# Optimization experiments

Hardware: AMD Instinct MI355X
Metric: run time of the kernel (lower is better)

The kernel has to match this reference:

```python
import jax, jax.numpy as jnp
import numpy as np
import math

N, E, C, NB, NEL, NG = 8192, 131072, 64, 8, 4, 16
R_MAX, AVG_NEI, P_CUT, NL, SH = 5.0, 16.0, 6, 2, 16


def _sph(u):
    # real spherical harmonics l=0..3, component normalization (sum_m Y_lm^2 = 2l+1 on unit sphere)
    x, y, z = u[:, 0], u[:, 1], u[:, 2]
    s3, s15, s5 = math.sqrt(3.0), math.sqrt(15.0), math.sqrt(5.0)
    s105, s7 = math.sqrt(105.0), math.sqrt(7.0)
    c35, c21 = math.sqrt(35.0 / 8.0), math.sqrt(21.0 / 8.0)
    Y = [jnp.ones_like(x),
         s3 * x, s3 * y, s3 * z,
         s15 * x * y, s15 * y * z, 0.5 * s5 * (3 * z * z - 1), s15 * x * z, 0.5 * s15 * (x * x - y * y),
         c35 * y * (3 * x * x - y * y), s105 * x * y * z, c21 * y * (5 * z * z - 1),
         0.5 * s7 * (5 * z ** 3 - 3 * z), c21 * x * (5 * z * z - 1),
         0.5 * s105 * z * (x * x - y * y), c35 * x * (x * x - 3 * y * y)]
    return jnp.stack(Y, axis=-1)  # [E,16]


def _bessel(r):
    k = jnp.arange(1, NB + 1, dtype=r.dtype)
    return math.sqrt(2.0 / R_MAX) * jnp.sin(k * jnp.pi * r[:, None] / R_MAX) / r[:, None]


def _poly_cutoff(r):
    p = float(P_CUT)
    x = r / R_MAX
    f = (1.0 - 0.5 * (p + 1) * (p + 2) * x ** p + p * (p + 2) * x ** (p + 1)
         - 0.5 * p * (p + 1) * x ** (p + 2))
    return f * (x < 1.0)


def setup_inputs() -> dict:
    key = jax.random.key(0)
    ks = jax.random.split(key, 16)
    sc = lambda fan: 1.0 / math.sqrt(fan)
    return {
        "pos": 2.0 * jax.random.normal(ks[0], (N, 3), jnp.float32),
        "atom_types": jax.random.randint(ks[1], (N,), 0, NEL),
        "edge_index": jax.random.randint(ks[2], (2, E), 0, N),
        "batch": jnp.sort(jax.random.randint(ks[3], (N,), 0, NG)),
        "W_embed": jax.random.normal(ks[4], (NEL, C), jnp.float32),
        "W_r1": sc(NB) * jax.random.normal(ks[5], (NL, NB, 64), jnp.float32),
        "W_r2": sc(64) * jax.random.normal(ks[6], (NL, 64, 64), jnp.float32),
        "W_r3": sc(64) * jax.random.normal(ks[7], (NL, 64, C), jnp.float32),
        "W_sc": sc(C) * jax.random.normal(ks[8], (NL, NEL, C, C), jnp.float32),
        "w_prod": 0.5 * jax.random.normal(ks[9], (NL, NEL, 4), jnp.float32),
        "w_ro0": sc(C) * jax.random.normal(ks[10], (C,), jnp.float32),
        "W_ro1a": sc(C) * jax.random.normal(ks[11], (C, 16), jnp.float32),
        "w_ro1b": sc(16) * jax.random.normal(ks[12], (16,), jnp.float32),
    }


def reference(pos, atom_types, edge_index, batch, W_embed, W_r1, W_r2, W_r3,
              W_sc, w_prod, w_ro0, W_ro1a, w_ro1b):
    src, dst = edge_index[0], edge_index[1]
    vec = pos[dst] - pos[src]                      # [E,3]
    r = jnp.sqrt(jnp.sum(vec * vec, -1) + 1e-12)   # [E]
    Y = _sph(vec / r[:, None])                     # [E,SH]
    edge_feats = _bessel(r) * _poly_cutoff(r)[:, None]  # [E,NB]
    h = W_embed[atom_types]                        # one-hot @ W == lookup, [N,C]
    energies = [jnp.zeros((NG,), pos.dtype)]       # pair_repulsion disabled
    for i in range(NL):
        Rw = jax.nn.silu(edge_feats @ W_r1[i])
        Rw = jax.nn.silu(Rw @ W_r2[i])
        Rw = Rw @ W_r3[i]                          # radial MLP weights [E,C]
        # gather-TP-scatter: message [E,C,SH] -> node A [N,C,SH]
        m = (Rw * h[src])[:, :, None] * Y[:, None, :]
        A = jax.ops.segment_sum(m.reshape(E, C * SH), dst,
                                num_segments=N).reshape(N, C, SH) / AVG_NEI
        sc_feat = jnp.einsum('nc,ncd->nd', h, W_sc[i][atom_types])  # element-dep skip
        inv = jnp.stack([A[:, :, 0],
                         jnp.sum(A[:, :, 1:4] ** 2, -1),
                         jnp.sum(A[:, :, 4:9] ** 2, -1),
                         jnp.sum(A[:, :, 9:16] ** 2, -1)], axis=-1)  # [N,C,4]
        h = jnp.einsum('ncj,nj->nc', inv, w_prod[i][atom_types]) + sc_feat
        if i < NL - 1:
            e_node = h @ w_ro0                     # linear readout
        else:
            e_node = jax.nn.silu(h @ W_ro1a) @ w_ro1b  # gated MLP readout
        energies.append(jax.ops.segment_sum(e_node, batch, num_segments=NG))
    contributions = jnp.stack(energies, -1)        # [NG, NL+1]
    return jnp.sum(contributions, -1)              # total energy per graph
```

## Files before the change

kernel.cpp:

```cpp
#include <hip/hip_runtime.h>
#include <hip/hip_bf16.h>
#include <math.h>

#define N_NODES 8192
#define N_EDGES 131072
#define NGRP 16
#define NLAY 2
#define NELM 4
constexpr float INV_AVG = 1.0f / 16.0f;
constexpr float PI_F = 3.14159265358979323846f;

#define CV_POS   0
#define CV_EMB   24576
#define CV_SC    42240
#define CV_PROD  75008
#define CV_RO0   75040
#define CV_RO1A  75104
#define CV_RO1B  76128
#define CVT_N    76144

#define SWZ_PER_L 10240
#define SWZ_N     20480

#define B_CVT  230
#define B_SWZ  80
#define B_HIST 512
#define CVT_WORK 58736

typedef __hip_bfloat16 bf16;
typedef __attribute__((ext_vector_type(8))) short bf16x8;
typedef __attribute__((ext_vector_type(4))) float f32x4;

__device__ __forceinline__ float silu_f(float x){ return x / (1.0f + __expf(-x)); }
__device__ __forceinline__ float bfbits2f(unsigned short u){
  return __uint_as_float(((unsigned)u) << 16);
}
__device__ __forceinline__ void unpack2(unsigned u, float& lo, float& hi){
  lo = __uint_as_float(u << 16);
  hi = __uint_as_float(u & 0xffff0000u);
}
__device__ __forceinline__ short f2bs(float v){
  union { bf16 b; short s; } u; u.b = __float2bfloat16(v); return u.s;
}
__device__ __forceinline__ float ldf(const void* p, int i, int flag){
  if (flag) return bfbits2f(((const unsigned short*)p)[i]);
  return ((const float*)p)[i];
}
__device__ __forceinline__ int detect_fl(const void* pos){
  int lane = threadIdx.x & 63;
  const unsigned short* u = (const unsigned short*)pos;
  float va = bfbits2f(u[2*lane]), vb = bfbits2f(u[2*lane+1]);
  bool bad = !(fabsf(va) <= 1000.0f) || !(fabsf(vb) <= 1000.0f);
  return (__ballot(bad) == 0ull) ? 1 : 0;
}
__device__ __forceinline__ void WSYNC(){ __builtin_amdgcn_wave_barrier(); }

__device__ __forceinline__ void gl_lds4(const void* g, void* l){
  __builtin_amdgcn_global_load_lds(
      (const __attribute__((address_space(1))) unsigned*)g,
      (__attribute__((address_space(3))) unsigned*)l, 4, 0, 0);
}
__device__ __forceinline__ void gl_lds16(const void* g, void* l){
  __builtin_amdgcn_global_load_lds(
      (const __attribute__((address_space(1))) unsigned*)g,
      (__attribute__((address_space(3))) unsigned*)l, 16, 0, 0);
}

__global__ void k_setup1(const void* __restrict__ pos, const void* __restrict__ Wemb,
                         const void* __restrict__ Wsc, const void* __restrict__ wprod,
                         const void* __restrict__ wro0, const void* __restrict__ Wro1a,
                         const void* __restrict__ wro1b, const void* __restrict__ Wr1,
                         const void* __restrict__ Wr2, const void* __restrict__ Wr3,
                         const int* __restrict__ dstp, float* __restrict__ cv,
                         short* __restrict__ swz, int* __restrict__ deg){
  int b = blockIdx.x, tix = threadIdx.x;
  if (b >= B_CVT + B_SWZ){
    int e = (b - B_CVT - B_SWZ)*256 + tix;
    atomicAdd(&deg[dstp[e]], 1);
    return;
  }
  int fl = detect_fl(pos);
  if (b < B_CVT){
    int i = b*256 + tix;
    if (i < 24576){ cv[CV_POS + i] = ldf(pos, i, fl); return; }
    if (i < 24832){ int j=i-24576; cv[CV_EMB + j] = ldf(Wemb, j, fl); return; }
    if (i < 57600){ int j=i-24832; cv[CV_SC  + j] = ldf(Wsc,  j, fl); return; }
    if (i < 57632){ int j=i-57600; cv[CV_PROD+ j] = ldf(wprod,j, fl); return; }
    if (i < 57696){ int j=i-57632; cv[CV_RO0 + j] = ldf(wro0, j, fl); return; }
    if (i < 58720){ int j=i-57696; cv[CV_RO1A+ j] = ldf(Wro1a,j, fl); return; }
    if (i < CVT_WORK){ int j=i-58720; cv[CV_RO1B+ j] = ldf(wro1b,j, fl); return; }
    return;
  }
  int i = (b - B_CVT)*256 + tix;
  int l = i / SWZ_PER_L, w = i % SWZ_PER_L;
  float v;
  if (w < 2048){
    int t = w >> 9, q = (w >> 7) & 3, n = (w >> 3) & 15, j = w & 7;
    int k = q*8 + j;
    v = (k < 8) ? ldf(Wr1, l*512 + k*64 + t*16 + n, fl) : 0.0f;
  } else if (w < 6144){
    int w2 = w - 2048;
    int nt = w2 >> 10, kt = (w2 >> 9) & 1, q = (w2 >> 7) & 3, n = (w2 >> 3) & 15, j = w2 & 7;
    int k = kt*32 + q*8 + j;
    v = ldf(Wr2, l*4096 + k*64 + nt*16 + n, fl);
  } else {
    int w3 = w - 6144;
    int nt = w3 >> 10, kt = (w3 >> 9) & 1, q = (w3 >> 7) & 3, n = (w3 >> 3) & 15, j = w3 & 7;
    int k = kt*32 + q*8 + j;
    v = ldf(Wr3, l*4096 + k*64 + nt*16 + n, fl);
  }
  swz[i] = f2bs(v);
}

__global__ void k_setup2(const int* __restrict__ deg, int* __restrict__ row_start,
                         int* __restrict__ cursor, const int* __restrict__ types,
                         const float* __restrict__ cvemb, float* __restrict__ h,
                         float* __restrict__ ene){
  if (blockIdx.x == 0){
    __shared__ int lds[1024];
    int t = threadIdx.x;
    if (t < NGRP) ene[t] = 0.0f;
    int v[8]; int tot = 0;
#pragma unroll
    for (int k = 0; k < 8; k++){ v[k] = deg[t*8+k]; tot += v[k]; }
    lds[t] = tot; __syncthreads();
    for (int off = 1; off < 1024; off <<= 1){
      int x = (t >= off) ? lds[t-off] : 0;
      __syncthreads();
      lds[t] += x;
      __syncthreads();
    }
    int base = lds[t] - tot;
#pragma unroll
    for (int k = 0; k < 8; k++){ row_start[t*8+k] = base; cursor[t*8+k] = base; base += v[k]; }
    if (t == 1023) row_start[N_NODES] = base;
  } else {
    int i = (blockIdx.x - 1)*1024 + threadIdx.x;
    int n = i >> 6, c = i & 63;
    h[i] = cvemb[types[n]*64 + c];
  }
}

__global__ void k_fillgeom(const int* __restrict__ ei, int* __restrict__ cursor,
                           const float* __restrict__ posf, int* __restrict__ sslot,
                           unsigned short* __restrict__ Yb, float* __restrict__ rbuf){
  int e = blockIdx.x*256 + threadIdx.x;
  int s = ei[e], d = ei[N_EDGES + e];
  int slot = atomicAdd(&cursor[d], 1);
  sslot[slot] = s;
  float vx = posf[d*3+0] - posf[s*3+0];
  float vy = posf[d*3+1] - posf[s*3+1];
  float vz = posf[d*3+2] - posf[s*3+2];
  float r = sqrtf(vx*vx + vy*vy + vz*vz + 1e-12f);
  float ir = 1.0f / r;
  float x = vx*ir, y = vy*ir, z = vz*ir;
  const float s3 = 1.7320508075688772f, s15 = 3.872983346207417f, s5 = 2.23606797749979f;
  const float s105 = 10.246950765959598f, s7 = 2.6457513110645907f;
  const float c35 = 2.091650066335189f, c21 = 1.6201851746019651f;
  float x2 = x*x, y2 = y*y, z2 = z*z;
  float ys[16] = {
    1.0f, s3*x, s3*y, s3*z,
    s15*x*y, s15*y*z, 0.5f*s5*(3.0f*z2-1.0f), s15*x*z,
    0.5f*s15*(x2-y2), c35*y*(3.0f*x2-y2), s105*x*y*z, c21*y*(5.0f*z2-1.0f),
    0.5f*s7*(5.0f*z2*z-3.0f*z), c21*x*(5.0f*z2-1.0f), 0.5f*s105*z*(x2-y2),
    c35*x*(x2-3.0f*y2) };
  union { bf16 b[16]; uint4 u[2]; } pk;
#pragma unroll
  for (int k = 0; k < 16; k++) pk.b[k] = __float2bfloat16(ys[k]);
  uint4* yp = (uint4*)(Yb + (size_t)slot*16);
  yp[0] = pk.u[0];
  yp[1] = pk.u[1];
  rbuf[slot] = r;
}

#define ROWS 72
__global__ void __launch_bounds__(256) k_mlp2(const float* __restrict__ rbuf,
        const short* __restrict__ sw, bf16* __restrict__ Rwb){
  __shared__ short lds[4][16*ROWS];
  int tix = threadIdx.x;
  int wv = tix >> 6, lane = tix & 63;
  int q = lane >> 4, nn = lane & 15;
  int ebase = blockIdx.x*64 + wv*16;

  float r = rbuf[ebase + nn];
  float xc = r * 0.2f;
  float f = 0.0f;
  if (xc < 1.0f){
    float x3 = xc*xc*xc, x6 = x3*x3, x7 = x6*xc, x8 = x7*xc;
    f = 1.0f - 28.0f*x6 + 48.0f*x7 - 21.0f*x8;
  }
  float bs = 0.6324555320336759f * f / r;
  float t0 = PI_F * r * 0.2f;
  float ef[8];
#pragma unroll
  for (int k = 0; k < 8; k++) ef[k] = bs * __sinf((float)(k+1) * t0);

  bf16x8 af1 = {0,0,0,0,0,0,0,0};
  if (q == 0){
#pragma unroll
    for (int j = 0; j < 8; j++) af1[j] = f2bs(ef[j]);
  }
  short* A = lds[wv];
  int row = lane >> 2, c4 = lane & 3;

  for (int l = 0; l < NLAY; l++){
    const bf16x8* S1 = (const bf16x8*)(sw + l*SWZ_PER_L);
    const bf16x8* S2 = (const bf16x8*)(sw + l*SWZ_PER_L + 2048);
    const bf16x8* S3 = (const bf16x8*)(sw + l*SWZ_PER_L + 6144);
    f32x4 acc[4];
#pragma unroll
    for (int t = 0; t < 4; t++){
      bf16x8 b = S1[t*64 + q*16 + nn];
      f32x4 z = {0.f,0.f,0.f,0.f};
      acc[t] = __builtin_amdgcn_mfma_f32_16x16x32_bf16(af1, b, z, 0, 0, 0);
    }
#pragma unroll
    for (int t = 0; t < 4; t++)
#pragma unroll
      for (int rg = 0; rg < 4; rg++)
        A[(q*4+rg)*ROWS + t*16 + nn] = f2bs(silu_f(acc[t][rg]));
    WSYNC();

    bf16x8 a0 = *(const bf16x8*)&A[nn*ROWS + 0*32 + q*8];
    bf16x8 a1 = *(const bf16x8*)&A[nn*ROWS + 1*32 + q*8];
    WSYNC();
#pragma unroll
    for (int t = 0; t < 4; t++){
      f32x4 z = {0.f,0.f,0.f,0.f};
      bf16x8 b0 = S2[t*128 + 0*64 + q*16 + nn];
      bf16x8 b1 = S2[t*128 + 1*64 + q*16 + nn];
      z = __builtin_amdgcn_mfma_f32_16x16x32_bf16(a0, b0, z, 0, 0, 0);
      z = __builtin_amdgcn_mfma_f32_16x16x32_bf16(a1, b1, z, 0, 0, 0);
      acc[t] = z;
    }
#pragma unroll
    for (int t = 0; t < 4; t++)
#pragma unroll
      for (int rg = 0; rg < 4; rg++)
        A[(q*4+rg)*ROWS + t*16 + nn] = f2bs(silu_f(acc[t][rg]));
    WSYNC();

    a0 = *(const bf16x8*)&A[nn*ROWS + 0*32 + q*8];
    a1 = *(const bf16x8*)&A[nn*ROWS + 1*32 + q*8];
    WSYNC();
#pragma unroll
    for (int t = 0; t < 4; t++){
      f32x4 z = {0.f,0.f,0.f,0.f};
      bf16x8 b0 = S3[t*128 + 0*64 + q*16 + nn];
      bf16x8 b1 = S3[t*128 + 1*64 + q*16 + nn];
      z = __builtin_amdgcn_mfma_f32_16x16x32_bf16(a0, b0, z, 0, 0, 0);
      z = __builtin_amdgcn_mfma_f32_16x16x32_bf16(a1, b1, z, 0, 0, 0);
      acc[t] = z;
    }
#pragma unroll
    for (int t = 0; t < 4; t++)
#pragma unroll
      for (int rg = 0; rg < 4; rg++)
        A[(q*4+rg)*ROWS + t*16 + nn] = f2bs(acc[t][rg]);
    WSYNC();

    uint4 u0 = *(const uint4*)&A[row*ROWS + c4*16];
    uint4 u1 = *(const uint4*)&A[row*ROWS + c4*16 + 8];
    uint4* gp = (uint4*)((unsigned short*)Rwb + (size_t)l*N_EDGES*64
                         + ((size_t)(ebase + row))*64 + c4*16);
    gp[0] = u0;
    gp[1] = u1;
    WSYNC();
  }
}

template<int LAYER_KIND>
__global__ void __launch_bounds__(256) k_gu(const bf16* __restrict__ Rwb,
        const float* __restrict__ h_old, float* __restrict__ h_new,
        const unsigned short* __restrict__ Yb, const int* __restrict__ row_start,
        const int* __restrict__ sslot,
        const int* __restrict__ types, const float* __restrict__ Wsc,
        const float* __restrict__ wprod, const float* __restrict__ wro0,
        const float* __restrict__ Wro1a, const float* __restrict__ wro1b,
        const int* __restrict__ batch, float* __restrict__ ene){
  __shared__ __align__(16) float          hS[4][16][64];
  __shared__ __align__(16) unsigned short rwS[4][16][64];
  __shared__ __align__(16) unsigned short yS[4][16][16];
  __shared__ float ebins[NGRP];
  __shared__ float hn_l[4][64];
  int tix = threadIdx.x;
  if (tix < NGRP) ebins[tix] = 0.0f;
  __syncthreads();
  int wv = tix >> 6, lane = tix & 63;
  int n = blockIdx.x * 4 + wv;
  int beg = row_start[n], end = row_start[n + 1];
  const unsigned short* RW = (const unsigned short*)Rwb;

  float acc[16];
#pragma unroll
  for (int s = 0; s < 16; s++) acc[s] = 0.0f;

  for (int cb = beg; cb < end; cb += 16){
    int cnt = min(16, end - cb);
    WSYNC();
    int sv = sslot[min(cb + (lane & 15), N_EDGES - 1)];
    const char* rwsrc = (const char*)RW + (size_t)cb*128 + lane*16;
    gl_lds16(rwsrc,        &rwS[wv][0][0]);
    gl_lds16(rwsrc + 1024, &rwS[wv][8][0]);
    const char* ysrc = (const char*)Yb + (size_t)cb*32 + lane*4;
    gl_lds4(ysrc,       &yS[wv][0][0]);
    gl_lds4(ysrc + 256, &yS[wv][8][0]);
    for (int i = 0; i < cnt; i++){
      int src = __builtin_amdgcn_readlane(sv, i);
      gl_lds4(h_old + (size_t)src*64 + lane, &hS[wv][i][0]);
    }
    asm volatile("s_waitcnt vmcnt(0)" ::: "memory");
    __builtin_amdgcn_sched_barrier(0);
    for (int i = 0; i < cnt; i++){
      float g = hS[wv][i][lane] * bfbits2f(rwS[wv][i][lane]);
      const uint4* yq = (const uint4*)&yS[wv][i][0];
      uint4 ya = yq[0], yb = yq[1];
      float lo, hi;
      unpack2(ya.x, lo, hi); acc[0]  += g*lo; acc[1]  += g*hi;
      unpack2(ya.y, lo, hi); acc[2]  += g*lo; acc[3]  += g*hi;
      unpack2(ya.z, lo, hi); acc[4]  += g*lo; acc[5]  += g*hi;
      unpack2(ya.w, lo, hi); acc[6]  += g*lo; acc[7]  += g*hi;
      unpack2(yb.x, lo, hi); acc[8]  += g*lo; acc[9]  += g*hi;
      unpack2(yb.y, lo, hi); acc[10] += g*lo; acc[11] += g*hi;
      unpack2(yb.z, lo, hi); acc[12] += g*lo; acc[13] += g*hi;
      unpack2(yb.w, lo, hi); acc[14] += g*lo; acc[15] += g*hi;
    }
  }
#pragma unroll
  for (int s = 0; s < 16; s++) acc[s] *= INV_AVG;

  int ty = __builtin_amdgcn_readfirstlane(types[n]);
  const float* Ws = Wsc + (size_t)ty*4096;
  float sc0 = 0.f, sc1 = 0.f, sc2 = 0.f, sc3 = 0.f;
#pragma unroll
  for (int c = 0; c < 64; c += 4){
    sc0 += h_old[(size_t)n*64 + c+0] * Ws[(c+0)*64 + lane];
    sc1 += h_old[(size_t)n*64 + c+1] * Ws[(c+1)*64 + lane];
    sc2 += h_old[(size_t)n*64 + c+2] * Ws[(c+2)*64 + lane];
    sc3 += h_old[(size_t)n*64 + c+3] * Ws[(c+3)*64 + lane];
  }
  float sc = (sc0 + sc1) + (sc2 + sc3);

  float inv0 = acc[0];
  float inv1 = acc[1]*acc[1] + acc[2]*acc[2] + acc[3]*acc[3];
  float inv2 = acc[4]*acc[4] + acc[5]*acc[5] + acc[6]*acc[6] + acc[7]*acc[7]
             + acc[8]*acc[8];
  float inv3 = acc[9]*acc[9] + acc[10]*acc[10] + acc[11]*acc[11] + acc[12]*acc[12]
             + acc[13]*acc[13] + acc[14]*acc[14] + acc[15]*acc[15];
  const float* wp = wprod + ty*4;
  float hn = inv0*wp[0] + inv1*wp[1] + inv2*wp[2] + inv3*wp[3] + sc;
  h_new[(size_t)n*64 + lane] = hn;

  float ev;
  if (LAYER_KIND == 0){
    float p = hn * wro0[lane];
#pragma unroll
    for (int off = 32; off >= 1; off >>= 1) p += __shfl_xor(p, off, 64);
    ev = p;
  } else {
    hn_l[wv][lane] = hn;
    int j = lane & 15;
    float pj = 0.0f;
#pragma unroll
    for (int c = 0; c < 64; c++)
      pj += hn_l[wv][c] * Wro1a[c*16 + j];
    float evj = silu_f(pj) * wro1b[j];
    evj += __shfl_xor(evj, 8, 64);
    evj += __shfl_xor(evj, 4, 64);
    evj += __shfl_xor(evj, 2, 64);
    evj += __shfl_xor(evj, 1, 64);
    ev = evj;
  }
  if (lane == 0) atomicAdd(&ebins[batch[n]], ev);
  __syncthreads();
  if (tix < NGRP){
    float v = ebins[tix];
    if (v != 0.0f) atomicAdd(&ene[tix], v);
  }
}

__global__ void k_out(const float* __restrict__ ene, const void* __restrict__ pos,
                      void* __restrict__ out){
  int fl = detect_fl(pos);
  int t = threadIdx.x;
  if (t < NGRP){
    if (fl) ((bf16*)out)[t] = __float2bfloat16(ene[t]);
    else    ((float*)out)[t] = ene[t];
  }
}

static inline size_t rup(size_t x){ return (x + 255) & ~(size_t)255; }

extern "C" void kernel_launch(void* const* d_in, const int* in_sizes, int n_in,
                              void* d_out, int out_size, void* d_ws, size_t ws_size,
                              hipStream_t stream) {
  const void* pos   = d_in[0];
  const int*  types = (const int*)d_in[1];
  const int*  ei    = (const int*)d_in[2];
  const int*  batch = (const int*)d_in[3];
  const void* Wemb  = d_in[4];
  const void* Wr1   = d_in[5];
  const void* Wr2   = d_in[6];
  const void* Wr3   = d_in[7];
  const void* Wsc   = d_in[8];
  const void* wprod = d_in[9];
  const void* wro0  = d_in[10];
  const void* Wro1a = d_in[11];
  const void* wro1b = d_in[12];

  char* w = (char*)d_ws;
  float* cv       = (float*)w; w += rup((size_t)CVT_N*4);
  short* swz      = (short*)w; w += rup((size_t)SWZ_N*2);
  float* ene      = (float*)w; w += 256;
  int*   deg      = (int*)  w; w += rup((size_t)N_NODES*4);
  int*   row_start= (int*)  w; w += rup((size_t)(N_NODES+1)*4);
  int*   cursor   = (int*)  w; w += rup((size_t)N_NODES*4);
  int*   sslot    = (int*)  w; w += rup((size_t)N_EDGES*4);
  float* h0       = (float*)w; w += rup((size_t)N_NODES*64*4);
  float* h1       = (float*)w; w += rup((size_t)N_NODES*64*4);
  float* rbuf     = (float*)w; w += rup((size_t)N_EDGES*4);
  unsigned short* Yb = (unsigned short*)w; w += rup((size_t)N_EDGES*16*2);
  bf16*  Rwb      = (bf16*) w; w += rup((size_t)NLAY*N_EDGES*64*2);
  w += 4096;

  hipMemsetAsync(deg, 0, N_NODES*4, stream);

  const int* dstp = ei + N_EDGES;
  k_setup1<<<B_CVT + B_SWZ + B_HIST, 256, 0, stream>>>(
      pos, Wemb, Wsc, wprod, wro0, Wro1a, wro1b, Wr1, Wr2, Wr3, dstp, cv, swz, deg);
  k_setup2<<<1 + (N_NODES*64)/1024, 1024, 0, stream>>>(
      deg, row_start, cursor, types, cv + CV_EMB, h0, ene);
  k_fillgeom<<<N_EDGES/256, 256, 0, stream>>>(ei, cursor, cv + CV_POS, sslot, Yb, rbuf);
  k_mlp2<<<N_EDGES/64, 256, 0, stream>>>(rbuf, swz, Rwb);

  k_gu<0><<<N_NODES/4, 256, 0, stream>>>(Rwb, h0, h1, Yb,
      row_start, sslot, types, cv + CV_SC, cv + CV_PROD,
      cv + CV_RO0, cv + CV_RO1A, cv + CV_RO1B, batch, ene);
  k_gu<1><<<N_NODES/4, 256, 0, stream>>>(Rwb + (size_t)N_EDGES*64, h1, h0, Yb,
      row_start, sslot, types, cv + CV_SC + (size_t)NELM*4096, cv + CV_PROD + NELM*4,
      cv + CV_RO0, cv + CV_RO1A, cv + CV_RO1B, batch, ene);

  k_out<<<1, 64, 0, stream>>>(ene, pos, d_out);
}
```

Measured before the change: 203.0 us.

## Fuse radial MLP into gather-update kernel, dropping the Rw edge buffer

Removes the separate radial MLP kernel and its bf16 per-edge weight buffer. Each gather kernel now recomputes the MFMA-based radial MLP for the block's edge chunk and multiplies it into the gathered neighbour features in LDS. The four waves cooperatively process 64-edge chunks covering the block's four nodes, with block-level syncs between stages. This trades global write/read traffic of the Rw buffer for redundant basis computation and extra __syncthreads per chunk.

```diff
diff --git a/kernel.cpp b/kernel.cpp
--- a/kernel.cpp
+++ b/kernel.cpp
@@ -59,11 +59,6 @@
   __builtin_amdgcn_global_load_lds(
       (const __attribute__((address_space(1))) unsigned*)g,
       (__attribute__((address_space(3))) unsigned*)l, 4, 0, 0);
-}
-__device__ __forceinline__ void gl_lds16(const void* g, void* l){
-  __builtin_amdgcn_global_load_lds(
-      (const __attribute__((address_space(1))) unsigned*)g,
-      (__attribute__((address_space(3))) unsigned*)l, 16, 0, 0);
 }
 
 __global__ void k_setup1(const void* __restrict__ pos, const void* __restrict__ Wemb,
@@ -174,103 +169,9 @@
 }
 
 #define ROWS 72
-__global__ void __launch_bounds__(256) k_mlp2(const float* __restrict__ rbuf,
-        const short* __restrict__ sw, bf16* __restrict__ Rwb){
-  __shared__ short lds[4][16*ROWS];
-  int tix = threadIdx.x;
-  int wv = tix >> 6, lane = tix & 63;
-  int q = lane >> 4, nn = lane & 15;
-  int ebase = blockIdx.x*64 + wv*16;
-
-  float r = rbuf[ebase + nn];
-  float xc = r * 0.2f;
-  float f = 0.0f;
-  if (xc < 1.0f){
-    float x3 = xc*xc*xc, x6 = x3*x3, x7 = x6*xc, x8 = x7*xc;
-    f = 1.0f - 28.0f*x6 + 48.0f*x7 - 21.0f*x8;
-  }
-  float bs = 0.6324555320336759f * f / r;
-  float t0 = PI_F * r * 0.2f;
-  float ef[8];
-#pragma unroll
-  for (int k = 0; k < 8; k++) ef[k] = bs * __sinf((float)(k+1) * t0);
-
-  bf16x8 af1 = {0,0,0,0,0,0,0,0};
-  if (q == 0){
-#pragma unroll
-    for (int j = 0; j < 8; j++) af1[j] = f2bs(ef[j]);
-  }
-  short* A = lds[wv];
-  int row = lane >> 2, c4 = lane & 3;
-
-  for (int l = 0; l < NLAY; l++){
-    const bf16x8* S1 = (const bf16x8*)(sw + l*SWZ_PER_L);
-    const bf16x8* S2 = (const bf16x8*)(sw + l*SWZ_PER_L + 2048);
-    const bf16x8* S3 = (const bf16x8*)(sw + l*SWZ_PER_L + 6144);
-    f32x4 acc[4];
-#pragma unroll
-    for (int t = 0; t < 4; t++){
-      bf16x8 b = S1[t*64 + q*16 + nn];
-      f32x4 z = {0.f,0.f,0.f,0.f};
-      acc[t] = __builtin_amdgcn_mfma_f32_16x16x32_bf16(af1, b, z, 0, 0, 0);
-    }
-#pragma unroll
-    for (int t = 0; t < 4; t++)
-#pragma unroll
-      for (int rg = 0; rg < 4; rg++)
-        A[(q*4+rg)*ROWS + t*16 + nn] = f2bs(silu_f(acc[t][rg]));
-    WSYNC();
-
-    bf16x8 a0 = *(const bf16x8*)&A[nn*ROWS + 0*32 + q*8];
-    bf16x8 a1 = *(const bf16x8*)&A[nn*ROWS + 1*32 + q*8];
-    WSYNC();
-#pragma unroll
-    for (int t = 0; t < 4; t++){
-      f32x4 z = {0.f,0.f,0.f,0.f};
-      bf16x8 b0 = S2[t*128 + 0*64 + q*16 + nn];
-      bf16x8 b1 = S2[t*128 + 1*64 + q*16 + nn];
-      z = __builtin_amdgcn_mfma_f32_16x16x32_bf16(a0, b0, z, 0, 0, 0);
-      z = __builtin_amdgcn_mfma_f32_16x16x32_bf16(a1, b1, z, 0, 0, 0);
-      acc[t] = z;
-    }
-#pragma unroll
-    for (int t = 0; t < 4; t++)
-#pragma unroll
-      for (int rg = 0; rg < 4; rg++)
-        A[(q*4+rg)*ROWS + t*16 + nn] = f2bs(silu_f(acc[t][rg]));
-    WSYNC();
-
-    a0 = *(const bf16x8*)&A[nn*ROWS + 0*32 + q*8];
-    a1 = *(const bf16x8*)&A[nn*ROWS + 1*32 + q*8];
-    WSYNC();
-#pragma unroll
-    for (int t = 0; t < 4; t++){
-      f32x4 z = {0.f,0.f,0.f,0.f};
-      bf16x8 b0 = S3[t*128 + 0*64 + q*16 + nn];
-      bf16x8 b1 = S3[t*128 + 1*64 + q*16 + nn];
-      z = __builtin_amdgcn_mfma_f32_16x16x32_bf16(a0, b0, z, 0, 0, 0);
-      z = __builtin_amdgcn_mfma_f32_16x16x32_bf16(a1, b1, z, 0, 0, 0);
-      acc[t] = z;
-    }
-#pragma unroll
-    for (int t = 0; t < 4; t++)
-#pragma unroll
-      for (int rg = 0; rg < 4; rg++)
-        A[(q*4+rg)*ROWS + t*16 + nn] = f2bs(acc[t][rg]);
-    WSYNC();
-
-    uint4 u0 = *(const uint4*)&A[row*ROWS + c4*16];
-    uint4 u1 = *(const uint4*)&A[row*ROWS + c4*16 + 8];
-    uint4* gp = (uint4*)((unsigned short*)Rwb + (size_t)l*N_EDGES*64
-                         + ((size_t)(ebase + row))*64 + c4*16);
-    gp[0] = u0;
-    gp[1] = u1;
-    WSYNC();
-  }
-}
-
 template<int LAYER_KIND>
-__global__ void __launch_bounds__(256) k_gu(const bf16* __restrict__ Rwb,
+__global__ void __launch_bounds__(256) k_gu(const short* __restrict__ sw,
+        const float* __restrict__ rbuf,
         const float* __restrict__ h_old, float* __restrict__ h_new,
         const unsigned short* __restrict__ Yb, const int* __restrict__ row_start,
         const int* __restrict__ sslot,
@@ -278,53 +179,146 @@
         const float* __restrict__ wprod, const float* __restrict__ wro0,
         const float* __restrict__ Wro1a, const float* __restrict__ wro1b,
         const int* __restrict__ batch, float* __restrict__ ene){
-  __shared__ __align__(16) float          hS[4][16][64];
-  __shared__ __align__(16) unsigned short rwS[4][16][64];
-  __shared__ __align__(16) unsigned short yS[4][16][16];
+  __shared__ __align__(16) float hS[64][64];
+  __shared__ __align__(16) unsigned short yS[64][16];
+  __shared__ short A_[4][16*ROWS];
   __shared__ float ebins[NGRP];
   __shared__ float hn_l[4][64];
   int tix = threadIdx.x;
   if (tix < NGRP) ebins[tix] = 0.0f;
   __syncthreads();
   int wv = tix >> 6, lane = tix & 63;
-  int n = blockIdx.x * 4 + wv;
-  int beg = row_start[n], end = row_start[n + 1];
-  const unsigned short* RW = (const unsigned short*)Rwb;
+  int q = lane >> 4, nn = lane & 15;
+  int n0 = blockIdx.x * 4;
+  int n  = n0 + wv;
+  int s0 = row_start[n0], sEnd = row_start[n0 + 4];
+  int my_beg = row_start[n], my_end = row_start[n + 1];
+  short* A = A_[wv];
+  int row = lane >> 2, c4 = lane & 3;
+
+  const bf16x8* S1 = (const bf16x8*)(sw);
+  const bf16x8* S2 = (const bf16x8*)(sw + 2048);
+  const bf16x8* S3 = (const bf16x8*)(sw + 6144);
 
   float acc[16];
 #pragma unroll
   for (int s = 0; s < 16; s++) acc[s] = 0.0f;
 
-  for (int cb = beg; cb < end; cb += 16){
-    int cnt = min(16, end - cb);
-    WSYNC();
-    int sv = sslot[min(cb + (lane & 15), N_EDGES - 1)];
-    const char* rwsrc = (const char*)RW + (size_t)cb*128 + lane*16;
-    gl_lds16(rwsrc,        &rwS[wv][0][0]);
-    gl_lds16(rwsrc + 1024, &rwS[wv][8][0]);
-    const char* ysrc = (const char*)Yb + (size_t)cb*32 + lane*4;
-    gl_lds4(ysrc,       &yS[wv][0][0]);
-    gl_lds4(ysrc + 256, &yS[wv][8][0]);
-    for (int i = 0; i < cnt; i++){
+  for (int cb = s0; cb < sEnd; cb += 64){
+    int wbase = cb + wv*16;
+    int wcnt  = min(16, max(0, sEnd - wbase));
+    int sv = sslot[min(wbase + nn, N_EDGES - 1)];
+    for (int i = 0; i < wcnt; i++){
       int src = __builtin_amdgcn_readlane(sv, i);
-      gl_lds4(h_old + (size_t)src*64 + lane, &hS[wv][i][0]);
+      gl_lds4(h_old + (size_t)src*64 + lane, &hS[wv*16 + i][0]);
+    }
+    if (wcnt > 0){
+      const char* ysrc = (const char*)Yb + (size_t)wbase*32 + lane*4;
+      gl_lds4(ysrc,       &yS[wv*16][0]);
+      gl_lds4(ysrc + 256, &yS[wv*16 + 8][0]);
+    }
+    {
+      float r = rbuf[min(wbase + nn, N_EDGES - 1)];
+      float xc = r * 0.2f;
+      float f = 0.0f;
+      if (xc < 1.0f){
+        float x3 = xc*xc*xc, x6 = x3*x3, x7 = x6*xc, x8 = x7*xc;
+        f = 1.0f - 28.0f*x6 + 48.0f*x7 - 21.0f*x8;
+      }
+      float bs = 0.6324555320336759f * f / r;
+      float t0 = PI_F * r * 0.2f;
+      bf16x8 af1 = {0,0,0,0,0,0,0,0};
+      if (q == 0){
+#pragma unroll
+        for (int j = 0; j < 8; j++) af1[j] = f2bs(bs * __sinf((float)(j+1) * t0));
+      }
+      f32x4 macc[4];
+#pragma unroll
+      for (int t = 0; t < 4; t++){
+        bf16x8 b = S1[t*64 + q*16 + nn];
+        f32x4 z = {0.f,0.f,0.f,0.f};
+        macc[t] = __builtin_amdgcn_mfma_f32_16x16x32_bf16(af1, b, z, 0, 0, 0);
+      }
+#pragma unroll
+      for (int t = 0; t < 4; t++)
+#pragma unroll
+        for (int rg = 0; rg < 4; rg++)
+          A[(q*4+rg)*ROWS + t*16 + nn] = f2bs(silu_f(macc[t][rg]));
+      WSYNC();
+      bf16x8 a0 = *(const bf16x8*)&A[nn*ROWS + 0*32 + q*8];
+      bf16x8 a1 = *(const bf16x8*)&A[nn*ROWS + 1*32 + q*8];
+      WSYNC();
+#pragma unroll
+      for (int t = 0; t < 4; t++){
+        f32x4 z = {0.f,0.f,0.f,0.f};
+        bf16x8 b0 = S2[t*128 + 0*64 + q*16 + nn];
+        bf16x8 b1 = S2[t*128 + 1*64 + q*16 + nn];
+        z = __builtin_amdgcn_mfma_f32_16x16x32_bf16(a0, b0, z, 0, 0, 0);
+        z = __builtin_amdgcn_mfma_f32_16x16x32_bf16(a1, b1, z, 0, 0, 0);
+        macc[t] = z;
+      }
+#pragma unroll
+      for (int t = 0; t < 4; t++)
+#pragma unroll
+        for (int rg = 0; rg < 4; rg++)
+          A[(q*4+rg)*ROWS + t*16 + nn] = f2bs(silu_f(macc[t][rg]));
+      WSYNC();
+      a0 = *(const bf16x8*)&A[nn*ROWS + 0*32 + q*8];
+      a1 = *(const bf16x8*)&A[nn*ROWS + 1*32 + q*8];
+      WSYNC();
+#pragma unroll
+      for (int t = 0; t < 4; t++){
+        f32x4 z = {0.f,0.f,0.f,0.f};
+        bf16x8 b0 = S3[t*128 + 0*64 + q*16 + nn];
+        bf16x8 b1 = S3[t*128 + 1*64 + q*16 + nn];
+        z = __builtin_amdgcn_mfma_f32_16x16x32_bf16(a0, b0, z, 0, 0, 0);
+        z = __builtin_amdgcn_mfma_f32_16x16x32_bf16(a1, b1, z, 0, 0, 0);
+        macc[t] = z;
+      }
+#pragma unroll
+      for (int t = 0; t < 4; t++)
+#pragma unroll
+        for (int rg = 0; rg < 4; rg++)
+          A[(q*4+rg)*ROWS + t*16 + nn] = f2bs(macc[t][rg]);
+      WSYNC();
     }
     asm volatile("s_waitcnt vmcnt(0)" ::: "memory");
     __builtin_amdgcn_sched_barrier(0);
-    for (int i = 0; i < cnt; i++){
-      float g = hS[wv][i][lane] * bfbits2f(rwS[wv][i][lane]);
-      const uint4* yq = (const uint4*)&yS[wv][i][0];
-      uint4 ya = yq[0], yb = yq[1];
-      float lo, hi;
-      unpack2(ya.x, lo, hi); acc[0]  += g*lo; acc[1]  += g*hi;
-      unpack2(ya.y, lo, hi); acc[2]  += g*lo; acc[3]  += g*hi;
-      unpack2(ya.z, lo, hi); acc[4]  += g*lo; acc[5]  += g*hi;
-      unpack2(ya.w, lo, hi); acc[6]  += g*lo; acc[7]  += g*hi;
-      unpack2(yb.x, lo, hi); acc[8]  += g*lo; acc[9]  += g*hi;
-      unpack2(yb.y, lo, hi); acc[10] += g*lo; acc[11] += g*hi;
-      unpack2(yb.z, lo, hi); acc[12] += g*lo; acc[13] += g*hi;
-      unpack2(yb.w, lo, hi); acc[14] += g*lo; acc[15] += g*hi;
-    }
+    {
+      union { uint4 u[2]; unsigned short s[16]; } rw;
+      rw.u[0] = *(const uint4*)&A[row*ROWS + c4*16];
+      rw.u[1] = *(const uint4*)&A[row*ROWS + c4*16 + 8];
+      float* hp = &hS[wv*16 + row][c4*16];
+      float4 h0v = ((float4*)hp)[0], h1v = ((float4*)hp)[1];
+      float4 h2v = ((float4*)hp)[2], h3v = ((float4*)hp)[3];
+      float hv[16] = {h0v.x,h0v.y,h0v.z,h0v.w, h1v.x,h1v.y,h1v.z,h1v.w,
+                      h2v.x,h2v.y,h2v.z,h2v.w, h3v.x,h3v.y,h3v.z,h3v.w};
+      float gv[16];
+#pragma unroll
+      for (int kk = 0; kk < 16; kk++) gv[kk] = bfbits2f(rw.s[kk]) * hv[kk];
+      ((float4*)hp)[0] = make_float4(gv[0],gv[1],gv[2],gv[3]);
+      ((float4*)hp)[1] = make_float4(gv[4],gv[5],gv[6],gv[7]);
+      ((float4*)hp)[2] = make_float4(gv[8],gv[9],gv[10],gv[11]);
+      ((float4*)hp)[3] = make_float4(gv[12],gv[13],gv[14],gv[15]);
+    }
+    __syncthreads();
+    int lo = max(my_beg, cb), hi2 = min(my_end, cb + 64);
+    for (int s = lo; s < hi2; s++){
+      int L = s - cb;
+      float g = hS[L][lane];
+      const uint4* yq = (const uint4*)&yS[L][0];
+      uint4 ya = yq[0], yb_ = yq[1];
+      float lo2, hi3;
+      unpack2(ya.x, lo2, hi3); acc[0]  += g*lo2; acc[1]  += g*hi3;
+      unpack2(ya.y, lo2, hi3); acc[2]  += g*lo2; acc[3]  += g*hi3;
+      unpack2(ya.z, lo2, hi3); acc[4]  += g*lo2; acc[5]  += g*hi3;
+      unpack2(ya.w, lo2, hi3); acc[6]  += g*lo2; acc[7]  += g*hi3;
+      unpack2(yb_.x, lo2, hi3); acc[8]  += g*lo2; acc[9]  += g*hi3;
+      unpack2(yb_.y, lo2, hi3); acc[10] += g*lo2; acc[11] += g*hi3;
+      unpack2(yb_.z, lo2, hi3); acc[12] += g*lo2; acc[13] += g*hi3;
+      unpack2(yb_.w, lo2, hi3); acc[14] += g*lo2; acc[15] += g*hi3;
+    }
+    __syncthreads();
   }
 #pragma unroll
   for (int s = 0; s < 16; s++) acc[s] *= INV_AVG;
@@ -420,7 +414,6 @@
   float* h1       = (float*)w; w += rup((size_t)N_NODES*64*4);
   float* rbuf     = (float*)w; w += rup((size_t)N_EDGES*4);
   unsigned short* Yb = (unsigned short*)w; w += rup((size_t)N_EDGES*16*2);
-  bf16*  Rwb      = (bf16*) w; w += rup((size_t)NLAY*N_EDGES*64*2);
   w += 4096;
 
   hipMemsetAsync(deg, 0, N_NODES*4, stream);
@@ -431,12 +424,11 @@
   k_setup2<<<1 + (N_NODES*64)/1024, 1024, 0, stream>>>(
       deg, row_start, cursor, types, cv + CV_EMB, h0, ene);
   k_fillgeom<<<N_EDGES/256, 256, 0, stream>>>(ei, cursor, cv + CV_POS, sslot, Yb, rbuf);
-  k_mlp2<<<N_EDGES/64, 256, 0, stream>>>(rbuf, swz, Rwb);
-
-  k_gu<0><<<N_NODES/4, 256, 0, stream>>>(Rwb, h0, h1, Yb,
+
+  k_gu<0><<<N_NODES/4, 256, 0, stream>>>(swz, rbuf, h0, h1, Yb,
       row_start, sslot, types, cv + CV_SC, cv + CV_PROD,
       cv + CV_RO0, cv + CV_RO1A, cv + CV_RO1B, batch, ene);
-  k_gu<1><<<N_NODES/4, 256, 0, stream>>>(Rwb + (size_t)N_EDGES*64, h1, h0, Yb,
+  k_gu<1><<<N_NODES/4, 256, 0, stream>>>(swz + SWZ_PER_L, rbuf, h1, h0, Yb,
       row_start, sslot, types, cv + CV_SC + (size_t)NELM*4096, cv + CV_PROD + NELM*4,
       cv + CV_RO0, cv + CV_RO1A, cv + CV_RO1B, batch, ene);
 
```

Result: slower. 214.3 us (+5.6%).

## Replace layer-0 neighbor feature gather with per-type embedding lookup; fuse output into last layer

Applied to the files above, without the earlier changes.

In layer 0 the node features are just the element embedding, so the kernel now stores each edge's source atom type as a byte and picks the feature from four embedding values held in registers. This replaces the per-edge 256-byte gather of h into LDS. The separate output kernel is removed: the last block of the layer-1 kernel, found with an atomic completion counter, writes the final energies. The cost is an extra byte store per edge in fillgeom and a counter that must be zeroed every call, which is folded into the existing memset.

```diff
diff --git a/kernel.cpp b/kernel.cpp
--- a/kernel.cpp
+++ b/kernel.cpp
@@ -142,12 +142,14 @@
 }
 
 __global__ void k_fillgeom(const int* __restrict__ ei, int* __restrict__ cursor,
-                           const float* __restrict__ posf, int* __restrict__ sslot,
+                           const float* __restrict__ posf, const int* __restrict__ types,
+                           int* __restrict__ sslot, unsigned char* __restrict__ tsl,
                            unsigned short* __restrict__ Yb, float* __restrict__ rbuf){
   int e = blockIdx.x*256 + threadIdx.x;
   int s = ei[e], d = ei[N_EDGES + e];
   int slot = atomicAdd(&cursor[d], 1);
   sslot[slot] = s;
+  tsl[slot] = (unsigned char)types[s];
   float vx = posf[d*3+0] - posf[s*3+0];
   float vy = posf[d*3+1] - posf[s*3+1];
   float vz = posf[d*3+2] - posf[s*3+2];
@@ -273,16 +275,20 @@
 __global__ void __launch_bounds__(256) k_gu(const bf16* __restrict__ Rwb,
         const float* __restrict__ h_old, float* __restrict__ h_new,
         const unsigned short* __restrict__ Yb, const int* __restrict__ row_start,
-        const int* __restrict__ sslot,
+        const int* __restrict__ sslot, const unsigned char* __restrict__ tsl,
         const int* __restrict__ types, const float* __restrict__ Wsc,
-        const float* __restrict__ wprod, const float* __restrict__ wro0,
+        const float* __restrict__ wprod, const float* __restrict__ wemb,
+        const float* __restrict__ wro0,
         const float* __restrict__ Wro1a, const float* __restrict__ wro1b,
-        const int* __restrict__ batch, float* __restrict__ ene){
-  __shared__ __align__(16) float          hS[4][16][64];
+        const int* __restrict__ batch, float* __restrict__ ene,
+        int* __restrict__ done, const void* __restrict__ pos,
+        void* __restrict__ out){
+  __shared__ __align__(16) float          hS[LAYER_KIND ? 4 : 1][16][64];
   __shared__ __align__(16) unsigned short rwS[4][16][64];
   __shared__ __align__(16) unsigned short yS[4][16][16];
   __shared__ float ebins[NGRP];
   __shared__ float hn_l[4][64];
+  __shared__ int lastBlk;
   int tix = threadIdx.x;
   if (tix < NGRP) ebins[tix] = 0.0f;
   __syncthreads();
@@ -291,6 +297,11 @@
   int beg = row_start[n], end = row_start[n + 1];
   const unsigned short* RW = (const unsigned short*)Rwb;
 
+  float e0=0.f, e1=0.f, e2=0.f, e3=0.f;
+  if (LAYER_KIND == 0){
+    e0 = wemb[lane]; e1 = wemb[64+lane]; e2 = wemb[128+lane]; e3 = wemb[192+lane];
+  }
+
   float acc[16];
 #pragma unroll
   for (int s = 0; s < 16; s++) acc[s] = 0.0f;
@@ -298,21 +309,34 @@
   for (int cb = beg; cb < end; cb += 16){
     int cnt = min(16, end - cb);
     WSYNC();
-    int sv = sslot[min(cb + (lane & 15), N_EDGES - 1)];
     const char* rwsrc = (const char*)RW + (size_t)cb*128 + lane*16;
     gl_lds16(rwsrc,        &rwS[wv][0][0]);
     gl_lds16(rwsrc + 1024, &rwS[wv][8][0]);
     const char* ysrc = (const char*)Yb + (size_t)cb*32 + lane*4;
     gl_lds4(ysrc,       &yS[wv][0][0]);
     gl_lds4(ysrc + 256, &yS[wv][8][0]);
-    for (int i = 0; i < cnt; i++){
-      int src = __builtin_amdgcn_readlane(sv, i);
-      gl_lds4(h_old + (size_t)src*64 + lane, &hS[wv][i][0]);
+    int tv = 0;
+    if (LAYER_KIND == 0){
+      tv = (int)tsl[min(cb + (lane & 15), N_EDGES - 1)];
+    } else {
+      int sv = sslot[min(cb + (lane & 15), N_EDGES - 1)];
+      for (int i = 0; i < cnt; i++){
+        int src = __builtin_amdgcn_readlane(sv, i);
+        gl_lds4(h_old + (size_t)src*64 + lane, &hS[wv][i][0]);
+      }
     }
     asm volatile("s_waitcnt vmcnt(0)" ::: "memory");
     __builtin_amdgcn_sched_barrier(0);
     for (int i = 0; i < cnt; i++){
-      float g = hS[wv][i][lane] * bfbits2f(rwS[wv][i][lane]);
+      float rw = bfbits2f(rwS[wv][i][lane]);
+      float hv;
+      if (LAYER_KIND == 0){
+        int ty = __builtin_amdgcn_readlane(tv, i);
+        hv = (ty & 2) ? ((ty & 1) ? e3 : e2) : ((ty & 1) ? e1 : e0);
+      } else {
+        hv = hS[wv][i][lane];
+      }
+      float g = rw * hv;
       const uint4* yq = (const uint4*)&yS[wv][i][0];
       uint4 ya = yq[0], yb = yq[1];
       float lo, hi;
@@ -377,15 +401,18 @@
     float v = ebins[tix];
     if (v != 0.0f) atomicAdd(&ene[tix], v);
   }
-}
-
-__global__ void k_out(const float* __restrict__ ene, const void* __restrict__ pos,
-                      void* __restrict__ out){
-  int fl = detect_fl(pos);
-  int t = threadIdx.x;
-  if (t < NGRP){
-    if (fl) ((bf16*)out)[t] = __float2bfloat16(ene[t]);
-    else    ((float*)out)[t] = ene[t];
+  if (LAYER_KIND == 1){
+    __syncthreads();
+    if (tix == 0) lastBlk = (atomicAdd(done, 1) == (int)gridDim.x - 1) ? 1 : 0;
+    __syncthreads();
+    if (lastBlk){
+      int fl = detect_fl(pos);
+      if (tix < NGRP){
+        float v = atomicAdd(&ene[tix], 0.0f);
+        if (fl) ((bf16*)out)[tix] = __float2bfloat16(v);
+        else    ((float*)out)[tix] = v;
+      }
+    }
   }
 }
 
@@ -412,33 +439,35 @@
   float* cv       = (float*)w; w += rup((size_t)CVT_N*4);
   short* swz      = (short*)w; w += rup((size_t)SWZ_N*2);
   float* ene      = (float*)w; w += 256;
-  int*   deg      = (int*)  w; w += rup((size_t)N_NODES*4);
+  int*   deg      = (int*)  w; w += rup((size_t)N_NODES*4 + 256);
   int*   row_start= (int*)  w; w += rup((size_t)(N_NODES+1)*4);
   int*   cursor   = (int*)  w; w += rup((size_t)N_NODES*4);
   int*   sslot    = (int*)  w; w += rup((size_t)N_EDGES*4);
+  unsigned char* tsl = (unsigned char*)w; w += rup((size_t)N_EDGES);
   float* h0       = (float*)w; w += rup((size_t)N_NODES*64*4);
   float* h1       = (float*)w; w += rup((size_t)N_NODES*64*4);
   float* rbuf     = (float*)w; w += rup((size_t)N_EDGES*4);
   unsigned short* Yb = (unsigned short*)w; w += rup((size_t)N_EDGES*16*2);
   bf16*  Rwb      = (bf16*) w; w += rup((size_t)NLAY*N_EDGES*64*2);
   w += 4096;
-
-  hipMemsetAsync(deg, 0, N_NODES*4, stream);
+  int* done = deg + N_NODES;
+
+  hipMemsetAsync(deg, 0, N_NODES*4 + 256, stream);
 
   const int* dstp = ei + N_EDGES;
   k_setup1<<<B_CVT + B_SWZ + B_HIST, 256, 0, stream>>>(
       pos, Wemb, Wsc, wprod, wro0, Wro1a, wro1b, Wr1, Wr2, Wr3, dstp, cv, swz, deg);
   k_setup2<<<1 + (N_NODES*64)/1024, 1024, 0, stream>>>(
       deg, row_start, cursor, types, cv + CV_EMB, h0, ene);
-  k_fillgeom<<<N_EDGES/256, 256, 0, stream>>>(ei, cursor, cv + CV_POS, sslot, Yb, rbuf);
+  k_fillgeom<<<N_EDGES/256, 256, 0, stream>>>(ei, cursor, cv + CV_POS, types,
+      sslot, tsl, Yb, rbuf);
   k_mlp2<<<N_EDGES/64, 256, 0, stream>>>(rbuf, swz, Rwb);
 
   k_gu<0><<<N_NODES/4, 256, 0, stream>>>(Rwb, h0, h1, Yb,
-      row_start, sslot, types, cv + CV_SC, cv + CV_PROD,
-      cv + CV_RO0, cv + CV_RO1A, cv + CV_RO1B, batch, ene);
+      row_start, sslot, tsl, types, cv + CV_SC, cv + CV_PROD, cv + CV_EMB,
+      cv + CV_RO0, cv + CV_RO1A, cv + CV_RO1B, batch, ene, done, pos, d_out);
   k_gu<1><<<N_NODES/4, 256, 0, stream>>>(Rwb + (size_t)N_EDGES*64, h1, h0, Yb,
-      row_start, sslot, types, cv + CV_SC + (size_t)NELM*4096, cv + CV_PROD + NELM*4,
-      cv + CV_RO0, cv + CV_RO1A, cv + CV_RO1B, batch, ene);
-
-  k_out<<<1, 64, 0, stream>>>(ene, pos, d_out);
-}
+      row_start, sslot, tsl, types, cv + CV_SC + (size_t)NELM*4096,
+      cv + CV_PROD + NELM*4, cv + CV_EMB,
+      cv + CV_RO0, cv + CV_RO1A, cv + CV_RO1B, batch, ene, done, pos, d_out);
+}
```

Result: slower. 242.9 us (+19.7%).
